# Performance work log

Hardware: AMD Instinct MI355X
Metric: run time of the kernel (lower is better)

## Reference

```python
import jax, jax.numpy as jnp
import numpy as np

N_NODES = 100000


def gcn_conv(x, src, dst, w, W, b, n):
    # PyG GCNConv: add self loops (weight 1), symmetric normalization,
    # linear transform, scatter-add aggregation, bias.
    loop = jnp.arange(n, dtype=src.dtype)
    s = jnp.concatenate([src, loop])
    d = jnp.concatenate([dst, loop])
    ew = jnp.concatenate([w, jnp.ones((n,), dtype=w.dtype)])
    deg = jax.ops.segment_sum(ew, d, num_segments=n)          # [N]
    dinv = jnp.where(deg > 0, jax.lax.rsqrt(deg), 0.0).astype(x.dtype)
    norm = dinv[s] * ew * dinv[d]                             # [E+N]
    h = x @ W                                                 # [N, out]
    msg = h[s] * norm[:, None]                                # gather + scale
    out = jax.ops.segment_sum(msg, d, num_segments=n)         # scatter-add
    return out + b


def setup_inputs() -> dict:
    key = jax.random.key(0)
    k1, k2, k3, k4, k5, k6 = jax.random.split(key, 6)
    n, e, c_in, c_hid, c_out = N_NODES, 1200000, 64, 64, 32
    node_matrix = jax.random.normal(k1, (n, c_in), dtype=jnp.float32)
    edge_index = jax.random.randint(k2, (2, e), 0, n, dtype=jnp.int64)
    edge_weights = jax.random.uniform(k3, (e,), dtype=jnp.float32)
    s_in = 1.0 / np.sqrt(c_in)
    s_hid = 1.0 / np.sqrt(c_hid)
    W1 = jax.random.uniform(k4, (c_in, c_hid), jnp.float32, -s_in, s_in)
    b1 = jnp.zeros((c_hid,), jnp.float32)
    W2 = jax.random.uniform(k5, (c_hid, c_out), jnp.float32, -s_hid, s_hid)
    b2 = jnp.zeros((c_out,), jnp.float32)
    return {"node_matrix": node_matrix, "edge_index": edge_index,
            "edge_weights": edge_weights, "W1": W1, "b1": b1, "W2": W2, "b2": b2}


def reference(node_matrix, edge_index, edge_weights, W1, b1, W2, b2):
    n = node_matrix.shape[0]
    src, dst = edge_index[0], edge_index[1]
    x = gcn_conv(node_matrix, src, dst, edge_weights, W1, b1, n)
    x = jax.nn.relu(x)
    x = gcn_conv(x, src, dst, edge_weights, W2, b2, n)
    return x
```

## Files before the change

kernel.cpp:

```cpp
#include <hip/hip_runtime.h>

static inline int ceil_div(long long a, long long b) { return (int)((a + b - 1) / b); }

#define RBITS 8
#define RNODES 256
#define CNT_BLOCKS 96
#define STAGE_CAP 4096

typedef __attribute__((ext_vector_type(8))) short bf16x8;
typedef __attribute__((ext_vector_type(4))) float f32x4;

__device__ inline unsigned f2bf(float f) {
    unsigned u = __float_as_uint(f);
    return (u + 0x7fffu + ((u >> 16) & 1u)) >> 16;
}
__device__ inline unsigned pack2(float a, float b) { return f2bf(a) | (f2bf(b) << 16); }
__device__ inline float bf2f(unsigned v) { return __uint_as_float(v << 16); }
__device__ inline float bf_lo(unsigned v) { return __uint_as_float(v << 16); }
__device__ inline float bf_hi(unsigned v) { return __uint_as_float(v & 0xffff0000u); }

__global__ void bin_count(const int* __restrict__ dst, int* __restrict__ hist_g,
                          int NB, int E) {
    __shared__ int hist[512];
    int t = threadIdx.x;
    hist[t] = 0;
    __syncthreads();
    int nvec = E >> 2;
    const int4* d4 = (const int4*)dst;
    for (int v = blockIdx.x * 512 + t; v < nvec; v += CNT_BLOCKS * 512) {
        int4 d = d4[v];
        atomicAdd(&hist[d.x >> RBITS], 1);
        atomicAdd(&hist[d.y >> RBITS], 1);
        atomicAdd(&hist[d.z >> RBITS], 1);
        atomicAdd(&hist[d.w >> RBITS], 1);
    }
    if (blockIdx.x == 0 && t < (E & 3))
        atomicAdd(&hist[dst[(nvec << 2) + t] >> RBITS], 1);
    __syncthreads();
    if (t < NB) hist_g[blockIdx.x * NB + t] = hist[t];
}

__global__ void bin_scan(const int* __restrict__ hist_g, int* __restrict__ bin_start,
                         int* __restrict__ bin_cursor, int NB) {
    __shared__ int s[512];
    int t = threadIdx.x;
    int v = 0;
    if (t < NB) {
        for (int k = 0; k < CNT_BLOCKS; ++k) v += hist_g[k * NB + t];
        bin_cursor[t] = 0;
    }
    s[t] = v;
    __syncthreads();
    for (int d = 1; d < 512; d <<= 1) {
        int a = (t >= d) ? s[t - d] : 0;
        __syncthreads();
        s[t] += a;
        __syncthreads();
    }
    if (t < NB) bin_start[t] = s[t] - v;
    if (t == NB - 1) bin_start[NB] = s[t];
}

#define SC_T 512
#define SC_K 8
#define SC_E (SC_T * SC_K)
__global__ void bin_scatter(const int* __restrict__ src, const int* __restrict__ dst,
                            const float* __restrict__ w, int* __restrict__ bin_cursor,
                            const int* __restrict__ bin_start,
                            int* __restrict__ bp, float* __restrict__ bw,
                            int NB, int E) {
    __shared__ int hist[512];
    __shared__ int offs[512];
    __shared__ int base[512];
    __shared__ int stage_p[SC_E];
    __shared__ float stage_w[SC_E];
    __shared__ unsigned short stage_b[SC_E];
    int t = threadIdx.x;
    hist[t] = 0;
    __syncthreads();
    int e0 = blockIdx.x * SC_E;
    int nE = E - e0; if (nE > SC_E) nE = SC_E;

    int myBin[SC_K], myRank[SC_K], myPack[SC_K];
    float myW[SC_K];
#pragma unroll
    for (int k = 0; k < SC_K; ++k) {
        int idx = t + k * SC_T;
        if (idx < nE) {
            int e = e0 + idx;
            int d = dst[e];
            int b = d >> RBITS;
            myBin[k] = b;
            myPack[k] = (src[e] << RBITS) | (d & (RNODES - 1));
            myW[k] = w[e];
            myRank[k] = atomicAdd(&hist[b], 1);
        }
    }
    __syncthreads();
    offs[t] = hist[t];
    __syncthreads();
    for (int d = 1; d < 512; d <<= 1) {
        int a = (t >= d) ? offs[t - d] : 0;
        __syncthreads();
        offs[t] += a;
        __syncthreads();
    }
    if (t < NB && hist[t]) base[t] = bin_start[t] + atomicAdd(&bin_cursor[t], hist[t]);
#pragma unroll
    for (int k = 0; k < SC_K; ++k) {
        int idx = t + k * SC_T;
        if (idx < nE) {
            int b = myBin[k];
            int pos = (offs[b] - hist[b]) + myRank[k];
            stage_p[pos] = myPack[k];
            stage_w[pos] = myW[k];
            stage_b[pos] = (unsigned short)b;
        }
    }
    __syncthreads();
    for (int p = t; p < nE; p += SC_T) {
        int b = stage_b[p];
        int g = base[b] + (p - (offs[b] - hist[b]));
        bp[g] = stage_p[p];
        bw[g] = stage_w[p];
    }
}

__global__ void csr_build(const int* __restrict__ bp, const float* __restrict__ bw,
                          const int* __restrict__ bin_start,
                          int* __restrict__ row_beg, int* __restrict__ row_cnt,
                          float* __restrict__ dinv, unsigned* __restrict__ ew, int N) {
    __shared__ int cnt[RNODES];
    __shared__ float wsum[RNODES];
    __shared__ int starts[RNODES];
    __shared__ int cur[RNODES];
    __shared__ int sp[STAGE_CAP];
    __shared__ float sw[STAGE_CAP];
    int b = blockIdx.x;
    int t = threadIdx.x;
    if (t < RNODES) { cnt[t] = 0; wsum[t] = 0.f; }
    __syncthreads();
    int beg = bin_start[b], end = bin_start[b + 1];
    int n = end - beg;
    for (int idx = t; idx < n; idx += 512) {
        int p = bp[beg + idx];
        float wv = bw[beg + idx];
        if (idx < STAGE_CAP) { sp[idx] = p; sw[idx] = wv; }
        atomicAdd(&cnt[p & (RNODES - 1)], 1);
        atomicAdd(&wsum[p & (RNODES - 1)], wv);
    }
    __syncthreads();
    if (t < RNODES) starts[t] = cnt[t];
    __syncthreads();
    for (int d = 1; d < RNODES; d <<= 1) {
        int a = 0;
        if (t < RNODES && t >= d) a = starts[t - d];
        __syncthreads();
        if (t < RNODES) starts[t] += a;
        __syncthreads();
    }
    if (t < RNODES) {
        int ex = starts[t] - cnt[t];
        cur[t] = beg + ex;
        int node = (b << RBITS) + t;
        if (node < N) {
            row_beg[node] = beg + ex;
            row_cnt[node] = cnt[t];
            dinv[node] = rsqrtf(wsum[t] + 1.0f);
        }
    }
    __syncthreads();
    for (int idx = t; idx < n; idx += 512) {
        int p;
        float wv;
        if (idx < STAGE_CAP) { p = sp[idx]; wv = sw[idx]; }
        else { p = bp[beg + idx]; wv = bw[beg + idx]; }
        int slot = atomicAdd(&cur[p & (RNODES - 1)], 1);
        ew[slot] = ((unsigned)(p >> RBITS) << 15) | (f2bf(wv) & 0x7fffu);
    }
}

__global__ __launch_bounds__(256) void gemm1_mfma(const float* __restrict__ X,
                                                  const float* __restrict__ W,
                                                  const float* __restrict__ dinv,
                                                  unsigned short* __restrict__ H, int N) {
    int lane = threadIdx.x & 63;
    int wv = threadIdx.x >> 6;
    int quad = lane >> 4;
    int col = lane & 15;

    bf16x8 Bh[4][2], Bl[4][2];
#pragma unroll
    for (int nt = 0; nt < 4; ++nt)
#pragma unroll
        for (int kh = 0; kh < 2; ++kh)
#pragma unroll
            for (int j = 0; j < 8; ++j) {
                float wval = W[(kh * 32 + quad * 8 + j) * 64 + nt * 16 + col];
                unsigned hb = f2bf(wval);
                Bh[nt][kh][j] = (short)hb;
                Bl[nt][kh][j] = (short)f2bf(wval - bf2f(hb));
            }

#pragma unroll
    for (int rt = 0; rt < 4; ++rt) {
        int rb = blockIdx.x * 256 + wv * 64 + rt * 16;
        if (rb >= N) break;
        int arow = rb + col;
        bf16x8 Ah[2], Al[2];
#pragma unroll
        for (int kh = 0; kh < 2; ++kh) {
            float xv[8];
            if (arow < N) {
                const float4* p = (const float4*)(X + (size_t)arow * 64 + kh * 32 + quad * 8);
                float4 f0 = p[0], f1 = p[1];
                xv[0] = f0.x; xv[1] = f0.y; xv[2] = f0.z; xv[3] = f0.w;
                xv[4] = f1.x; xv[5] = f1.y; xv[6] = f1.z; xv[7] = f1.w;
            } else {
#pragma unroll
                for (int j = 0; j < 8; ++j) xv[j] = 0.f;
            }
#pragma unroll
            for (int j = 0; j < 8; ++j) {
                unsigned hb = f2bf(xv[j]);
                Ah[kh][j] = (short)hb;
                Al[kh][j] = (short)f2bf(xv[j] - bf2f(hb));
            }
        }
        f32x4 acc[4] = {{0,0,0,0},{0,0,0,0},{0,0,0,0},{0,0,0,0}};
#pragma unroll
        for (int nt = 0; nt < 4; ++nt)
#pragma unroll
            for (int kh = 0; kh < 2; ++kh) {
                acc[nt] = __builtin_amdgcn_mfma_f32_16x16x32_bf16(Ah[kh], Bh[nt][kh], acc[nt], 0, 0, 0);
                acc[nt] = __builtin_amdgcn_mfma_f32_16x16x32_bf16(Al[kh], Bh[nt][kh], acc[nt], 0, 0, 0);
                acc[nt] = __builtin_amdgcn_mfma_f32_16x16x32_bf16(Ah[kh], Bl[nt][kh], acc[nt], 0, 0, 0);
            }
        float dval[4];
#pragma unroll
        for (int r = 0; r < 4; ++r) {
            int row = rb + quad * 4 + r;
            dval[r] = (row < N) ? dinv[row] : 0.f;
        }
#pragma unroll
        for (int nt = 0; nt < 4; ++nt)
#pragma unroll
            for (int r = 0; r < 4; ++r) {
                int row = rb + quad * 4 + r;
                if (row < N)
                    H[(size_t)row * 64 + nt * 16 + col] = (unsigned short)f2bf(acc[nt][r] * dval[r]);
            }
    }
}

__global__ __launch_bounds__(256) void gemm2_mfma(const unsigned short* __restrict__ Xb,
                                                  const float* __restrict__ W,
                                                  const float* __restrict__ dinv,
                                                  unsigned short* __restrict__ H, int N) {
    int lane = threadIdx.x & 63;
    int wv = threadIdx.x >> 6;
    int quad = lane >> 4;
    int col = lane & 15;

    bf16x8 Bh[2][2], Bl[2][2];
#pragma unroll
    for (int nt = 0; nt < 2; ++nt)
#pragma unroll
        for (int kh = 0; kh < 2; ++kh)
#pragma unroll
            for (int j = 0; j < 8; ++j) {
                float wval = W[(kh * 32 + quad * 8 + j) * 32 + nt * 16 + col];
                unsigned hb = f2bf(wval);
                Bh[nt][kh][j] = (short)hb;
                Bl[nt][kh][j] = (short)f2bf(wval - bf2f(hb));
            }

#pragma unroll
    for (int rt = 0; rt < 4; ++rt) {
        int rb = blockIdx.x * 256 + wv * 64 + rt * 16;
        if (rb >= N) break;
        int arow = rb + col;
        bf16x8 A[2];
#pragma unroll
        for (int kh = 0; kh < 2; ++kh) {
            if (arow < N) {
                const bf16x8* p = (const bf16x8*)(Xb + (size_t)arow * 64 + kh * 32 + quad * 8);
                A[kh] = *p;
            } else {
                A[kh] = bf16x8{0,0,0,0,0,0,0,0};
            }
        }
        f32x4 acc[2] = {{0,0,0,0},{0,0,0,0}};
#pragma unroll
        for (int nt = 0; nt < 2; ++nt)
#pragma unroll
            for (int kh = 0; kh < 2; ++kh) {
                acc[nt] = __builtin_amdgcn_mfma_f32_16x16x32_bf16(A[kh], Bh[nt][kh], acc[nt], 0, 0, 0);
                acc[nt] = __builtin_amdgcn_mfma_f32_16x16x32_bf16(A[kh], Bl[nt][kh], acc[nt], 0, 0, 0);
            }
        float dval[4];
#pragma unroll
        for (int r = 0; r < 4; ++r) {
            int row = rb + quad * 4 + r;
            dval[r] = (row < N) ? dinv[row] : 0.f;
        }
#pragma unroll
        for (int nt = 0; nt < 2; ++nt)
#pragma unroll
            for (int r = 0; r < 4; ++r) {
                int row = rb + quad * 4 + r;
                if (row < N)
                    H[(size_t)row * 32 + nt * 16 + col] = (unsigned short)f2bf(acc[nt][r] * dval[r]);
            }
    }
}

__global__ void aggregate64(const unsigned* __restrict__ g, const int* __restrict__ row_beg,
                            const int* __restrict__ row_cnt, const unsigned* __restrict__ ew,
                            const float* __restrict__ dinv, const float* __restrict__ b,
                            unsigned* __restrict__ outb, int N) {
    int t = threadIdx.x;
    int c = t & 7;
    int i = blockIdx.x * 64 + (t >> 3);
    if (i >= N) return;
    int e = row_beg[i];
    int end = e + row_cnt[i];
    const uint4* h4 = (const uint4*)g;
    float acc[8];
#pragma unroll
    for (int j = 0; j < 8; ++j) acc[j] = 0.f;
    for (; e + 3 < end; e += 4) {
        unsigned e0 = ew[e], e1 = ew[e + 1], e2 = ew[e + 2], e3 = ew[e + 3];
        float n0 = __uint_as_float((e0 & 0x7fffu) << 16);
        float n1 = __uint_as_float((e1 & 0x7fffu) << 16);
        float n2 = __uint_as_float((e2 & 0x7fffu) << 16);
        float n3 = __uint_as_float((e3 & 0x7fffu) << 16);
        uint4 v0 = h4[(size_t)(e0 >> 15) * 8 + c];
        uint4 v1 = h4[(size_t)(e1 >> 15) * 8 + c];
        uint4 v2 = h4[(size_t)(e2 >> 15) * 8 + c];
        uint4 v3 = h4[(size_t)(e3 >> 15) * 8 + c];
        acc[0] += n0 * bf_lo(v0.x) + n1 * bf_lo(v1.x) + n2 * bf_lo(v2.x) + n3 * bf_lo(v3.x);
        acc[1] += n0 * bf_hi(v0.x) + n1 * bf_hi(v1.x) + n2 * bf_hi(v2.x) + n3 * bf_hi(v3.x);
        acc[2] += n0 * bf_lo(v0.y) + n1 * bf_lo(v1.y) + n2 * bf_lo(v2.y) + n3 * bf_lo(v3.y);
        acc[3] += n0 * bf_hi(v0.y) + n1 * bf_hi(v1.y) + n2 * bf_hi(v2.y) + n3 * bf_hi(v3.y);
        acc[4] += n0 * bf_lo(v0.z) + n1 * bf_lo(v1.z) + n2 * bf_lo(v2.z) + n3 * bf_lo(v3.z);
        acc[5] += n0 * bf_hi(v0.z) + n1 * bf_hi(v1.z) + n2 * bf_hi(v2.z) + n3 * bf_hi(v3.z);
        acc[6] += n0 * bf_lo(v0.w) + n1 * bf_lo(v1.w) + n2 * bf_lo(v2.w) + n3 * bf_lo(v3.w);
        acc[7] += n0 * bf_hi(v0.w) + n1 * bf_hi(v1.w) + n2 * bf_hi(v2.w) + n3 * bf_hi(v3.w);
    }
    for (; e < end; ++e) {
        unsigned e0 = ew[e];
        float n0 = __uint_as_float((e0 & 0x7fffu) << 16);
        uint4 v0 = h4[(size_t)(e0 >> 15) * 8 + c];
        acc[0] += n0 * bf_lo(v0.x);
        acc[1] += n0 * bf_hi(v0.x);
        acc[2] += n0 * bf_lo(v0.y);
        acc[3] += n0 * bf_hi(v0.y);
        acc[4] += n0 * bf_lo(v0.z);
        acc[5] += n0 * bf_hi(v0.z);
        acc[6] += n0 * bf_lo(v0.w);
        acc[7] += n0 * bf_hi(v0.w);
    }
    float di = dinv[i];
    uint4 hv = h4[(size_t)i * 8 + c];
    float hs[8] = {bf_lo(hv.x), bf_hi(hv.x), bf_lo(hv.y), bf_hi(hv.y),
                   bf_lo(hv.z), bf_hi(hv.z), bf_lo(hv.w), bf_hi(hv.w)};
    float4 b0 = ((const float4*)b)[c * 2];
    float4 b1 = ((const float4*)b)[c * 2 + 1];
    float o[8];
    o[0] = b0.x + di * (hs[0] + acc[0]);
    o[1] = b0.y + di * (hs[1] + acc[1]);
    o[2] = b0.z + di * (hs[2] + acc[2]);
    o[3] = b0.w + di * (hs[3] + acc[3]);
    o[4] = b1.x + di * (hs[4] + acc[4]);
    o[5] = b1.y + di * (hs[5] + acc[5]);
    o[6] = b1.z + di * (hs[6] + acc[6]);
    o[7] = b1.w + di * (hs[7] + acc[7]);
#pragma unroll
    for (int j = 0; j < 8; ++j) o[j] = fmaxf(o[j], 0.f);
    uint4 ov;
    ov.x = pack2(o[0], o[1]);
    ov.y = pack2(o[2], o[3]);
    ov.z = pack2(o[4], o[5]);
    ov.w = pack2(o[6], o[7]);
    ((uint4*)outb)[(size_t)i * 8 + c] = ov;
}

__global__ void aggregate32(const unsigned* __restrict__ g, const int* __restrict__ row_beg,
                            const int* __restrict__ row_cnt, const unsigned* __restrict__ ew,
                            const float* __restrict__ dinv, const float* __restrict__ b,
                            float* __restrict__ out, int N) {
    int t = threadIdx.x;
    int c = t & 3;
    int i = blockIdx.x * 128 + (t >> 2);
    if (i >= N) return;
    int e = row_beg[i];
    int end = e + row_cnt[i];
    const uint4* h4 = (const uint4*)g;
    float acc[8];
#pragma unroll
    for (int j = 0; j < 8; ++j) acc[j] = 0.f;
    for (; e + 3 < end; e += 4) {
        unsigned e0 = ew[e], e1 = ew[e + 1], e2 = ew[e + 2], e3 = ew[e + 3];
        float n0 = __uint_as_float((e0 & 0x7fffu) << 16);
        float n1 = __uint_as_float((e1 & 0x7fffu) << 16);
        float n2 = __uint_as_float((e2 & 0x7fffu) << 16);
        float n3 = __uint_as_float((e3 & 0x7fffu) << 16);
        uint4 v0 = h4[(size_t)(e0 >> 15) * 4 + c];
        uint4 v1 = h4[(size_t)(e1 >> 15) * 4 + c];
        uint4 v2 = h4[(size_t)(e2 >> 15) * 4 + c];
        uint4 v3 = h4[(size_t)(e3 >> 15) * 4 + c];
        acc[0] += n0 * bf_lo(v0.x) + n1 * bf_lo(v1.x) + n2 * bf_lo(v2.x) + n3 * bf_lo(v3.x);
        acc[1] += n0 * bf_hi(v0.x) + n1 * bf_hi(v1.x) + n2 * bf_hi(v2.x) + n3 * bf_hi(v3.x);
        acc[2] += n0 * bf_lo(v0.y) + n1 * bf_lo(v1.y) + n2 * bf_lo(v2.y) + n3 * bf_lo(v3.y);
        acc[3] += n0 * bf_hi(v0.y) + n1 * bf_hi(v1.y) + n2 * bf_hi(v2.y) + n3 * bf_hi(v3.y);
        acc[4] += n0 * bf_lo(v0.z) + n1 * bf_lo(v1.z) + n2 * bf_lo(v2.z) + n3 * bf_lo(v3.z);
        acc[5] += n0 * bf_hi(v0.z) + n1 * bf_hi(v1.z) + n2 * bf_hi(v2.z) + n3 * bf_hi(v3.z);
        acc[6] += n0 * bf_lo(v0.w) + n1 * bf_lo(v1.w) + n2 * bf_lo(v2.w) + n3 * bf_lo(v3.w);
        acc[7] += n0 * bf_hi(v0.w) + n1 * bf_hi(v1.w) + n2 * bf_hi(v2.w) + n3 * bf_hi(v3.w);
    }
    for (; e < end; ++e) {
        unsigned e0 = ew[e];
        float n0 = __uint_as_float((e0 & 0x7fffu) << 16);
        uint4 v0 = h4[(size_t)(e0 >> 15) * 4 + c];
        acc[0] += n0 * bf_lo(v0.x);
        acc[1] += n0 * bf_hi(v0.x);
        acc[2] += n0 * bf_lo(v0.y);
        acc[3] += n0 * bf_hi(v0.y);
        acc[4] += n0 * bf_lo(v0.z);
        acc[5] += n0 * bf_hi(v0.z);
        acc[6] += n0 * bf_lo(v0.w);
        acc[7] += n0 * bf_hi(v0.w);
    }
    float di = dinv[i];
    uint4 hv = h4[(size_t)i * 4 + c];
    float hs[8] = {bf_lo(hv.x), bf_hi(hv.x), bf_lo(hv.y), bf_hi(hv.y),
                   bf_lo(hv.z), bf_hi(hv.z), bf_lo(hv.w), bf_hi(hv.w)};
    float4 b0 = ((const float4*)b)[c * 2];
    float4 b1 = ((const float4*)b)[c * 2 + 1];
    float4 o0, o1;
    o0.x = b0.x + di * (hs[0] + acc[0]);
    o0.y = b0.y + di * (hs[1] + acc[1]);
    o0.z = b0.z + di * (hs[2] + acc[2]);
    o0.w = b0.w + di * (hs[3] + acc[3]);
    o1.x = b1.x + di * (hs[4] + acc[4]);
    o1.y = b1.y + di * (hs[5] + acc[5]);
    o1.z = b1.z + di * (hs[6] + acc[6]);
    o1.w = b1.w + di * (hs[7] + acc[7]);
    float4* op = (float4*)(out + (size_t)i * 32 + c * 8);
    op[0] = o0;
    op[1] = o1;
}

extern "C" void kernel_launch(void* const* d_in, const int* in_sizes, int n_in,
                              void* d_out, int out_size, void* d_ws, size_t ws_size,
                              hipStream_t stream) {
    const float* x  = (const float*)d_in[0];
    const int* eidx = (const int*)d_in[1];
    const float* w  = (const float*)d_in[2];
    const float* W1 = (const float*)d_in[3];
    const float* b1 = (const float*)d_in[4];
    const float* W2 = (const float*)d_in[5];
    const float* b2 = (const float*)d_in[6];
    float* out = (float*)d_out;

    const int E = in_sizes[2];
    const int N = in_sizes[0] / 64;
    const int* src = eidx;
    const int* dst = eidx + E;
    const int NB = ceil_div(N, RNODES);

    char* ws = (char*)d_ws;
    size_t off = 0;
    auto alloc = [&](size_t bytes) -> void* {
        void* p = ws + off;
        off = (off + bytes + 255) & ~(size_t)255;
        return p;
    };
    int*      hist_g     = (int*)alloc((size_t)CNT_BLOCKS * NB * 4);
    int*      bin_cursor = (int*)alloc((size_t)NB * 4);
    int*      bin_start  = (int*)alloc((size_t)(NB + 1) * 4);
    int*      bp         = (int*)alloc((size_t)E * 4);
    float*    bw         = (float*)alloc((size_t)E * 4);
    unsigned* ew         = (unsigned*)alloc((size_t)E * 4);
    int*      row_beg    = (int*)alloc((size_t)N * 4);
    int*      row_cnt    = (int*)alloc((size_t)N * 4);
    float*    dinv       = (float*)alloc((size_t)N * 4);
    unsigned* g1         = (unsigned*)alloc((size_t)N * 32 * 4);
    unsigned* out1b      = (unsigned*)alloc((size_t)N * 32 * 4);
    unsigned* g2         = (unsigned*)alloc((size_t)N * 16 * 4);

    bin_count<<<CNT_BLOCKS, 512, 0, stream>>>(dst, hist_g, NB, E);
    bin_scan<<<1, 512, 0, stream>>>(hist_g, bin_start, bin_cursor, NB);
    bin_scatter<<<ceil_div(E, SC_E), SC_T, 0, stream>>>(src, dst, w, bin_cursor, bin_start,
                                                        bp, bw, NB, E);
    csr_build<<<NB, 512, 0, stream>>>(bp, bw, bin_start, row_beg, row_cnt, dinv, ew, N);

    gemm1_mfma<<<ceil_div(N, 256), 256, 0, stream>>>(x, W1, dinv, (unsigned short*)g1, N);
    aggregate64<<<ceil_div(N, 64), 512, 0, stream>>>(g1, row_beg, row_cnt, ew, dinv, b1, out1b, N);

    gemm2_mfma<<<ceil_div(N, 256), 256, 0, stream>>>((const unsigned short*)out1b, W2, dinv,
                                                     (unsigned short*)g2, N);
    aggregate32<<<ceil_div(N, 128), 512, 0, stream>>>(g2, row_beg, row_cnt, ew, dinv, b2, out, N);
}
```

Baseline: 204.3 us.

## Process two nodes per thread group in aggregation kernels; drop csr_build LDS staging

Both aggregation kernels now assign two destination rows to each thread group and interleave their edge loops, issuing eight independent gathers per iteration instead of four. The aim is more memory-level parallelism to hide gather latency, at the cost of half as many launched threads and more registers. Separately, csr_build drops its shared-memory staging of bin entries and re-reads bp/bw from global memory in the second pass, which frees LDS and may raise occupancy but adds global traffic.

```diff
diff --git a/kernel.cpp b/kernel.cpp
--- a/kernel.cpp
+++ b/kernel.cpp
@@ -5,7 +5,6 @@
 #define RBITS 8
 #define RNODES 256
 #define CNT_BLOCKS 96
-#define STAGE_CAP 4096
 
 typedef __attribute__((ext_vector_type(8))) short bf16x8;
 typedef __attribute__((ext_vector_type(4))) float f32x4;
@@ -18,6 +17,20 @@
 __device__ inline float bf2f(unsigned v) { return __uint_as_float(v << 16); }
 __device__ inline float bf_lo(unsigned v) { return __uint_as_float(v << 16); }
 __device__ inline float bf_hi(unsigned v) { return __uint_as_float(v & 0xffff0000u); }
+
+#define ACC8(acc, n, v)                      \
+    do {                                     \
+        acc[0] += (n) * bf_lo((v).x);        \
+        acc[1] += (n) * bf_hi((v).x);        \
+        acc[2] += (n) * bf_lo((v).y);        \
+        acc[3] += (n) * bf_hi((v).y);        \
+        acc[4] += (n) * bf_lo((v).z);        \
+        acc[5] += (n) * bf_hi((v).z);        \
+        acc[6] += (n) * bf_lo((v).w);        \
+        acc[7] += (n) * bf_hi((v).w);        \
+    } while (0)
+
+#define EWN(e) __uint_as_float(((e) & 0x7fffu) << 16)
 
 __global__ void bin_count(const int* __restrict__ dst, int* __restrict__ hist_g,
                           int NB, int E) {
@@ -134,20 +147,15 @@
     __shared__ float wsum[RNODES];
     __shared__ int starts[RNODES];
     __shared__ int cur[RNODES];
-    __shared__ int sp[STAGE_CAP];
-    __shared__ float sw[STAGE_CAP];
     int b = blockIdx.x;
     int t = threadIdx.x;
     if (t < RNODES) { cnt[t] = 0; wsum[t] = 0.f; }
     __syncthreads();
     int beg = bin_start[b], end = bin_start[b + 1];
-    int n = end - beg;
-    for (int idx = t; idx < n; idx += 512) {
-        int p = bp[beg + idx];
-        float wv = bw[beg + idx];
-        if (idx < STAGE_CAP) { sp[idx] = p; sw[idx] = wv; }
+    for (int e = beg + t; e < end; e += 512) {
+        int p = bp[e];
         atomicAdd(&cnt[p & (RNODES - 1)], 1);
-        atomicAdd(&wsum[p & (RNODES - 1)], wv);
+        atomicAdd(&wsum[p & (RNODES - 1)], bw[e]);
     }
     __syncthreads();
     if (t < RNODES) starts[t] = cnt[t];
@@ -170,13 +178,10 @@
         }
     }
     __syncthreads();
-    for (int idx = t; idx < n; idx += 512) {
-        int p;
-        float wv;
-        if (idx < STAGE_CAP) { p = sp[idx]; wv = sw[idx]; }
-        else { p = bp[beg + idx]; wv = bw[beg + idx]; }
+    for (int e = beg + t; e < end; e += 512) {
+        int p = bp[e];
         int slot = atomicAdd(&cur[p & (RNODES - 1)], 1);
-        ew[slot] = ((unsigned)(p >> RBITS) << 15) | (f2bf(wv) & 0x7fffu);
+        ew[slot] = ((unsigned)(p >> RBITS) << 15) | (f2bf(bw[e]) & 0x7fffu);
     }
 }
 
@@ -321,69 +326,102 @@
                             unsigned* __restrict__ outb, int N) {
     int t = threadIdx.x;
     int c = t & 7;
-    int i = blockIdx.x * 64 + (t >> 3);
-    if (i >= N) return;
-    int e = row_beg[i];
-    int end = e + row_cnt[i];
+    int i0 = blockIdx.x * 128 + (t >> 3) * 2;
+    if (i0 >= N) return;
+    int i1 = i0 + 1;
+    bool hasB = i1 < N;
+    int eA = row_beg[i0], endA = eA + row_cnt[i0];
+    int eB = hasB ? row_beg[i1] : 0;
+    int endB = hasB ? eB + row_cnt[i1] : 0;
     const uint4* h4 = (const uint4*)g;
-    float acc[8];
-#pragma unroll
-    for (int j = 0; j < 8; ++j) acc[j] = 0.f;
-    for (; e + 3 < end; e += 4) {
-        unsigned e0 = ew[e], e1 = ew[e + 1], e2 = ew[e + 2], e3 = ew[e + 3];
-        float n0 = __uint_as_float((e0 & 0x7fffu) << 16);
-        float n1 = __uint_as_float((e1 & 0x7fffu) << 16);
-        float n2 = __uint_as_float((e2 & 0x7fffu) << 16);
-        float n3 = __uint_as_float((e3 & 0x7fffu) << 16);
-        uint4 v0 = h4[(size_t)(e0 >> 15) * 8 + c];
-        uint4 v1 = h4[(size_t)(e1 >> 15) * 8 + c];
-        uint4 v2 = h4[(size_t)(e2 >> 15) * 8 + c];
-        uint4 v3 = h4[(size_t)(e3 >> 15) * 8 + c];
-        acc[0] += n0 * bf_lo(v0.x) + n1 * bf_lo(v1.x) + n2 * bf_lo(v2.x) + n3 * bf_lo(v3.x);
-        acc[1] += n0 * bf_hi(v0.x) + n1 * bf_hi(v1.x) + n2 * bf_hi(v2.x) + n3 * bf_hi(v3.x);
-        acc[2] += n0 * bf_lo(v0.y) + n1 * bf_lo(v1.y) + n2 * bf_lo(v2.y) + n3 * bf_lo(v3.y);
-        acc[3] += n0 * bf_hi(v0.y) + n1 * bf_hi(v1.y) + n2 * bf_hi(v2.y) + n3 * bf_hi(v3.y);
-        acc[4] += n0 * bf_lo(v0.z) + n1 * bf_lo(v1.z) + n2 * bf_lo(v2.z) + n3 * bf_lo(v3.z);
-        acc[5] += n0 * bf_hi(v0.z) + n1 * bf_hi(v1.z) + n2 * bf_hi(v2.z) + n3 * bf_hi(v3.z);
-        acc[6] += n0 * bf_lo(v0.w) + n1 * bf_lo(v1.w) + n2 * bf_lo(v2.w) + n3 * bf_lo(v3.w);
-        acc[7] += n0 * bf_hi(v0.w) + n1 * bf_hi(v1.w) + n2 * bf_hi(v2.w) + n3 * bf_hi(v3.w);
-    }
-    for (; e < end; ++e) {
-        unsigned e0 = ew[e];
-        float n0 = __uint_as_float((e0 & 0x7fffu) << 16);
-        uint4 v0 = h4[(size_t)(e0 >> 15) * 8 + c];
-        acc[0] += n0 * bf_lo(v0.x);
-        acc[1] += n0 * bf_hi(v0.x);
-        acc[2] += n0 * bf_lo(v0.y);
-        acc[3] += n0 * bf_hi(v0.y);
-        acc[4] += n0 * bf_lo(v0.z);
-        acc[5] += n0 * bf_hi(v0.z);
-        acc[6] += n0 * bf_lo(v0.w);
-        acc[7] += n0 * bf_hi(v0.w);
-    }
-    float di = dinv[i];
-    uint4 hv = h4[(size_t)i * 8 + c];
-    float hs[8] = {bf_lo(hv.x), bf_hi(hv.x), bf_lo(hv.y), bf_hi(hv.y),
-                   bf_lo(hv.z), bf_hi(hv.z), bf_lo(hv.w), bf_hi(hv.w)};
-    float4 b0 = ((const float4*)b)[c * 2];
-    float4 b1 = ((const float4*)b)[c * 2 + 1];
-    float o[8];
-    o[0] = b0.x + di * (hs[0] + acc[0]);
-    o[1] = b0.y + di * (hs[1] + acc[1]);
-    o[2] = b0.z + di * (hs[2] + acc[2]);
-    o[3] = b0.w + di * (hs[3] + acc[3]);
-    o[4] = b1.x + di * (hs[4] + acc[4]);
-    o[5] = b1.y + di * (hs[5] + acc[5]);
-    o[6] = b1.z + di * (hs[6] + acc[6]);
-    o[7] = b1.w + di * (hs[7] + acc[7]);
-#pragma unroll
-    for (int j = 0; j < 8; ++j) o[j] = fmaxf(o[j], 0.f);
-    uint4 ov;
-    ov.x = pack2(o[0], o[1]);
-    ov.y = pack2(o[2], o[3]);
-    ov.z = pack2(o[4], o[5]);
-    ov.w = pack2(o[6], o[7]);
-    ((uint4*)outb)[(size_t)i * 8 + c] = ov;
+    float accA[8], accB[8];
+#pragma unroll
+    for (int j = 0; j < 8; ++j) { accA[j] = 0.f; accB[j] = 0.f; }
+    while (eA + 3 < endA && eB + 3 < endB) {
+        unsigned a0 = ew[eA], a1 = ew[eA + 1], a2 = ew[eA + 2], a3 = ew[eA + 3];
+        unsigned b0 = ew[eB], b1 = ew[eB + 1], b2 = ew[eB + 2], b3 = ew[eB + 3];
+        uint4 va0 = h4[(size_t)(a0 >> 15) * 8 + c];
+        uint4 va1 = h4[(size_t)(a1 >> 15) * 8 + c];
+        uint4 va2 = h4[(size_t)(a2 >> 15) * 8 + c];
+        uint4 va3 = h4[(size_t)(a3 >> 15) * 8 + c];
+        uint4 vb0 = h4[(size_t)(b0 >> 15) * 8 + c];
+        uint4 vb1 = h4[(size_t)(b1 >> 15) * 8 + c];
+        uint4 vb2 = h4[(size_t)(b2 >> 15) * 8 + c];
+        uint4 vb3 = h4[(size_t)(b3 >> 15) * 8 + c];
+        ACC8(accA, EWN(a0), va0); ACC8(accA, EWN(a1), va1);
+        ACC8(accA, EWN(a2), va2); ACC8(accA, EWN(a3), va3);
+        ACC8(accB, EWN(b0), vb0); ACC8(accB, EWN(b1), vb1);
+        ACC8(accB, EWN(b2), vb2); ACC8(accB, EWN(b3), vb3);
+        eA += 4; eB += 4;
+    }
+    for (; eA + 3 < endA; eA += 4) {
+        unsigned a0 = ew[eA], a1 = ew[eA + 1], a2 = ew[eA + 2], a3 = ew[eA + 3];
+        uint4 va0 = h4[(size_t)(a0 >> 15) * 8 + c];
+        uint4 va1 = h4[(size_t)(a1 >> 15) * 8 + c];
+        uint4 va2 = h4[(size_t)(a2 >> 15) * 8 + c];
+        uint4 va3 = h4[(size_t)(a3 >> 15) * 8 + c];
+        ACC8(accA, EWN(a0), va0); ACC8(accA, EWN(a1), va1);
+        ACC8(accA, EWN(a2), va2); ACC8(accA, EWN(a3), va3);
+    }
+    for (; eA < endA; ++eA) {
+        unsigned a0 = ew[eA];
+        uint4 va0 = h4[(size_t)(a0 >> 15) * 8 + c];
+        ACC8(accA, EWN(a0), va0);
+    }
+    for (; eB + 3 < endB; eB += 4) {
+        unsigned b0 = ew[eB], b1 = ew[eB + 1], b2 = ew[eB + 2], b3 = ew[eB + 3];
+        uint4 vb0 = h4[(size_t)(b0 >> 15) * 8 + c];
+        uint4 vb1 = h4[(size_t)(b1 >> 15) * 8 + c];
+        uint4 vb2 = h4[(size_t)(b2 >> 15) * 8 + c];
+        uint4 vb3 = h4[(size_t)(b3 >> 15) * 8 + c];
+        ACC8(accB, EWN(b0), vb0); ACC8(accB, EWN(b1), vb1);
+        ACC8(accB, EWN(b2), vb2); ACC8(accB, EWN(b3), vb3);
+    }
+    for (; eB < endB; ++eB) {
+        unsigned b0 = ew[eB];
+        uint4 vb0 = h4[(size_t)(b0 >> 15) * 8 + c];
+        ACC8(accB, EWN(b0), vb0);
+    }
+    const float4* b4 = (const float4*)b;
+    float4 bv0 = b4[c * 2];
+    float4 bv1 = b4[c * 2 + 1];
+    float bb[8] = {bv0.x, bv0.y, bv0.z, bv0.w, bv1.x, bv1.y, bv1.z, bv1.w};
+    {
+        float di = dinv[i0];
+        uint4 hv = h4[(size_t)i0 * 8 + c];
+        float hs[8] = {bf_lo(hv.x), bf_hi(hv.x), bf_lo(hv.y), bf_hi(hv.y),
+                       bf_lo(hv.z), bf_hi(hv.z), bf_lo(hv.w), bf_hi(hv.w)};
+        uint4 ov;
+        float o0 = fmaxf(bb[0] + di * (hs[0] + accA[0]), 0.f);
+        float o1 = fmaxf(bb[1] + di * (hs[1] + accA[1]), 0.f);
+        float o2 = fmaxf(bb[2] + di * (hs[2] + accA[2]), 0.f);
+        float o3 = fmaxf(bb[3] + di * (hs[3] + accA[3]), 0.f);
+        float o4 = fmaxf(bb[4] + di * (hs[4] + accA[4]), 0.f);
+        float o5 = fmaxf(bb[5] + di * (hs[5] + accA[5]), 0.f);
+        float o6 = fmaxf(bb[6] + di * (hs[6] + accA[6]), 0.f);
+        float o7 = fmaxf(bb[7] + di * (hs[7] + accA[7]), 0.f);
+        ov.x = pack2(o0, o1); ov.y = pack2(o2, o3);
+        ov.z = pack2(o4, o5); ov.w = pack2(o6, o7);
+        ((uint4*)outb)[(size_t)i0 * 8 + c] = ov;
+    }
+    if (hasB) {
+        float di = dinv[i1];
+        uint4 hv = h4[(size_t)i1 * 8 + c];
+        float hs[8] = {bf_lo(hv.x), bf_hi(hv.x), bf_lo(hv.y), bf_hi(hv.y),
+                       bf_lo(hv.z), bf_hi(hv.z), bf_lo(hv.w), bf_hi(hv.w)};
+        uint4 ov;
+        float o0 = fmaxf(bb[0] + di * (hs[0] + accB[0]), 0.f);
+        float o1 = fmaxf(bb[1] + di * (hs[1] + accB[1]), 0.f);
+        float o2 = fmaxf(bb[2] + di * (hs[2] + accB[2]), 0.f);
+        float o3 = fmaxf(bb[3] + di * (hs[3] + accB[3]), 0.f);
+        float o4 = fmaxf(bb[4] + di * (hs[4] + accB[4]), 0.f);
+        float o5 = fmaxf(bb[5] + di * (hs[5] + accB[5]), 0.f);
+        float o6 = fmaxf(bb[6] + di * (hs[6] + accB[6]), 0.f);
+        float o7 = fmaxf(bb[7] + di * (hs[7] + accB[7]), 0.f);
+        ov.x = pack2(o0, o1); ov.y = pack2(o2, o3);
+        ov.z = pack2(o4, o5); ov.w = pack2(o6, o7);
+        ((uint4*)outb)[(size_t)i1 * 8 + c] = ov;
+    }
 }
 
 __global__ void aggregate32(const unsigned* __restrict__ g, const int* __restrict__ row_beg,
@@ -392,64 +430,102 @@
                             float* __restrict__ out, int N) {
     int t = threadIdx.x;
     int c = t & 3;
-    int i = blockIdx.x * 128 + (t >> 2);
-    if (i >= N) return;
-    int e = row_beg[i];
-    int end = e + row_cnt[i];
+    int i0 = blockIdx.x * 256 + (t >> 2) * 2;
+    if (i0 >= N) return;
+    int i1 = i0 + 1;
+    bool hasB = i1 < N;
+    int eA = row_beg[i0], endA = eA + row_cnt[i0];
+    int eB = hasB ? row_beg[i1] : 0;
+    int endB = hasB ? eB + row_cnt[i1] : 0;
     const uint4* h4 = (const uint4*)g;
-    float acc[8];
-#pragma unroll
-    for (int j = 0; j < 8; ++j) acc[j] = 0.f;
-    for (; e + 3 < end; e += 4) {
-        unsigned e0 = ew[e], e1 = ew[e + 1], e2 = ew[e + 2], e3 = ew[e + 3];
-        float n0 = __uint_as_float((e0 & 0x7fffu) << 16);
-        float n1 = __uint_as_float((e1 & 0x7fffu) << 16);
-        float n2 = __uint_as_float((e2 & 0x7fffu) << 16);
-        float n3 = __uint_as_float((e3 & 0x7fffu) << 16);
-        uint4 v0 = h4[(size_t)(e0 >> 15) * 4 + c];
-        uint4 v1 = h4[(size_t)(e1 >> 15) * 4 + c];
-        uint4 v2 = h4[(size_t)(e2 >> 15) * 4 + c];
-        uint4 v3 = h4[(size_t)(e3 >> 15) * 4 + c];
-        acc[0] += n0 * bf_lo(v0.x) + n1 * bf_lo(v1.x) + n2 * bf_lo(v2.x) + n3 * bf_lo(v3.x);
-        acc[1] += n0 * bf_hi(v0.x) + n1 * bf_hi(v1.x) + n2 * bf_hi(v2.x) + n3 * bf_hi(v3.x);
-        acc[2] += n0 * bf_lo(v0.y) + n1 * bf_lo(v1.y) + n2 * bf_lo(v2.y) + n3 * bf_lo(v3.y);
-        acc[3] += n0 * bf_hi(v0.y) + n1 * bf_hi(v1.y) + n2 * bf_hi(v2.y) + n3 * bf_hi(v3.y);
-        acc[4] += n0 * bf_lo(v0.z) + n1 * bf_lo(v1.z) + n2 * bf_lo(v2.z) + n3 * bf_lo(v3.z);
-        acc[5] += n0 * bf_hi(v0.z) + n1 * bf_hi(v1.z) + n2 * bf_hi(v2.z) + n3 * bf_hi(v3.z);
-        acc[6] += n0 * bf_lo(v0.w) + n1 * bf_lo(v1.w) + n2 * bf_lo(v2.w) + n3 * bf_lo(v3.w);
-        acc[7] += n0 * bf_hi(v0.w) + n1 * bf_hi(v1.w) + n2 * bf_hi(v2.w) + n3 * bf_hi(v3.w);
-    }
-    for (; e < end; ++e) {
-        unsigned e0 = ew[e];
-        float n0 = __uint_as_float((e0 & 0x7fffu) << 16);
-        uint4 v0 = h4[(size_t)(e0 >> 15) * 4 + c];
-        acc[0] += n0 * bf_lo(v0.x);
-        acc[1] += n0 * bf_hi(v0.x);
-        acc[2] += n0 * bf_lo(v0.y);
-        acc[3] += n0 * bf_hi(v0.y);
-        acc[4] += n0 * bf_lo(v0.z);
-        acc[5] += n0 * bf_hi(v0.z);
-        acc[6] += n0 * bf_lo(v0.w);
-        acc[7] += n0 * bf_hi(v0.w);
-    }
-    float di = dinv[i];
-    uint4 hv = h4[(size_t)i * 4 + c];
-    float hs[8] = {bf_lo(hv.x), bf_hi(hv.x), bf_lo(hv.y), bf_hi(hv.y),
-                   bf_lo(hv.z), bf_hi(hv.z), bf_lo(hv.w), bf_hi(hv.w)};
-    float4 b0 = ((const float4*)b)[c * 2];
-    float4 b1 = ((const float4*)b)[c * 2 + 1];
-    float4 o0, o1;
-    o0.x = b0.x + di * (hs[0] + acc[0]);
-    o0.y = b0.y + di * (hs[1] + acc[1]);
-    o0.z = b0.z + di * (hs[2] + acc[2]);
-    o0.w = b0.w + di * (hs[3] + acc[3]);
-    o1.x = b1.x + di * (hs[4] + acc[4]);
-    o1.y = b1.y + di * (hs[5] + acc[5]);
-    o1.z = b1.z + di * (hs[6] + acc[6]);
-    o1.w = b1.w + di * (hs[7] + acc[7]);
-    float4* op = (float4*)(out + (size_t)i * 32 + c * 8);
-    op[0] = o0;
-    op[1] = o1;
+    float accA[8], accB[8];
+#pragma unroll
+    for (int j = 0; j < 8; ++j) { accA[j] = 0.f; accB[j] = 0.f; }
+    while (eA + 3 < endA && eB + 3 < endB) {
+        unsigned a0 = ew[eA], a1 = ew[eA + 1], a2 = ew[eA + 2], a3 = ew[eA + 3];
+        unsigned b0 = ew[eB], b1 = ew[eB + 1], b2 = ew[eB + 2], b3 = ew[eB + 3];
+        uint4 va0 = h4[(size_t)(a0 >> 15) * 4 + c];
+        uint4 va1 = h4[(size_t)(a1 >> 15) * 4 + c];
+        uint4 va2 = h4[(size_t)(a2 >> 15) * 4 + c];
+        uint4 va3 = h4[(size_t)(a3 >> 15) * 4 + c];
+        uint4 vb0 = h4[(size_t)(b0 >> 15) * 4 + c];
+        uint4 vb1 = h4[(size_t)(b1 >> 15) * 4 + c];
+        uint4 vb2 = h4[(size_t)(b2 >> 15) * 4 + c];
+        uint4 vb3 = h4[(size_t)(b3 >> 15) * 4 + c];
+        ACC8(accA, EWN(a0), va0); ACC8(accA, EWN(a1), va1);
+        ACC8(accA, EWN(a2), va2); ACC8(accA, EWN(a3), va3);
+        ACC8(accB, EWN(b0), vb0); ACC8(accB, EWN(b1), vb1);
+        ACC8(accB, EWN(b2), vb2); ACC8(accB, EWN(b3), vb3);
+        eA += 4; eB += 4;
+    }
+    for (; eA + 3 < endA; eA += 4) {
+        unsigned a0 = ew[eA], a1 = ew[eA + 1], a2 = ew[eA + 2], a3 = ew[eA + 3];
+        uint4 va0 = h4[(size_t)(a0 >> 15) * 4 + c];
+        uint4 va1 = h4[(size_t)(a1 >> 15) * 4 + c];
+        uint4 va2 = h4[(size_t)(a2 >> 15) * 4 + c];
+        uint4 va3 = h4[(size_t)(a3 >> 15) * 4 + c];
+        ACC8(accA, EWN(a0), va0); ACC8(accA, EWN(a1), va1);
+        ACC8(accA, EWN(a2), va2); ACC8(accA, EWN(a3), va3);
+    }
+    for (; eA < endA; ++eA) {
+        unsigned a0 = ew[eA];
+        uint4 va0 = h4[(size_t)(a0 >> 15) * 4 + c];
+        ACC8(accA, EWN(a0), va0);
+    }
+    for (; eB + 3 < endB; eB += 4) {
+        unsigned b0 = ew[eB], b1 = ew[eB + 1], b2 = ew[eB + 2], b3 = ew[eB + 3];
+        uint4 vb0 = h4[(size_t)(b0 >> 15) * 4 + c];
+        uint4 vb1 = h4[(size_t)(b1 >> 15) * 4 + c];
+        uint4 vb2 = h4[(size_t)(b2 >> 15) * 4 + c];
+        uint4 vb3 = h4[(size_t)(b3 >> 15) * 4 + c];
+        ACC8(accB, EWN(b0), vb0); ACC8(accB, EWN(b1), vb1);
+        ACC8(accB, EWN(b2), vb2); ACC8(accB, EWN(b3), vb3);
+    }
+    for (; eB < endB; ++eB) {
+        unsigned b0 = ew[eB];
+        uint4 vb0 = h4[(size_t)(b0 >> 15) * 4 + c];
+        ACC8(accB, EWN(b0), vb0);
+    }
+    const float4* b4 = (const float4*)b;
+    float4 bv0 = b4[c * 2];
+    float4 bv1 = b4[c * 2 + 1];
+    float bb[8] = {bv0.x, bv0.y, bv0.z, bv0.w, bv1.x, bv1.y, bv1.z, bv1.w};
+    {
+        float di = dinv[i0];
+        uint4 hv = h4[(size_t)i0 * 4 + c];
+        float hs[8] = {bf_lo(hv.x), bf_hi(hv.x), bf_lo(hv.y), bf_hi(hv.y),
+                       bf_lo(hv.z), bf_hi(hv.z), bf_lo(hv.w), bf_hi(hv.w)};
+        float4 o0, o1;
+        o0.x = bb[0] + di * (hs[0] + accA[0]);
+        o0.y = bb[1] + di * (hs[1] + accA[1]);
+        o0.z = bb[2] + di * (hs[2] + accA[2]);
+        o0.w = bb[3] + di * (hs[3] + accA[3]);
+        o1.x = bb[4] + di * (hs[4] + accA[4]);
+        o1.y = bb[5] + di * (hs[5] + accA[5]);
+        o1.z = bb[6] + di * (hs[6] + accA[6]);
+        o1.w = bb[7] + di * (hs[7] + accA[7]);
+        float4* op = (float4*)(out + (size_t)i0 * 32 + c * 8);
+        op[0] = o0;
+        op[1] = o1;
+    }
+    if (hasB) {
+        float di = dinv[i1];
+        uint4 hv = h4[(size_t)i1 * 4 + c];
+        float hs[8] = {bf_lo(hv.x), bf_hi(hv.x), bf_lo(hv.y), bf_hi(hv.y),
+                       bf_lo(hv.z), bf_hi(hv.z), bf_lo(hv.w), bf_hi(hv.w)};
+        float4 o0, o1;
+        o0.x = bb[0] + di * (hs[0] + accB[0]);
+        o0.y = bb[1] + di * (hs[1] + accB[1]);
+        o0.z = bb[2] + di * (hs[2] + accB[2]);
+        o0.w = bb[3] + di * (hs[3] + accB[3]);
+        o1.x = bb[4] + di * (hs[4] + accB[4]);
+        o1.y = bb[5] + di * (hs[5] + accB[5]);
+        o1.z = bb[6] + di * (hs[6] + accB[6]);
+        o1.w = bb[7] + di * (hs[7] + accB[7]);
+        float4* op = (float4*)(out + (size_t)i1 * 32 + c * 8);
+        op[0] = o0;
+        op[1] = o1;
+    }
 }
 
 extern "C" void kernel_launch(void* const* d_in, const int* in_sizes, int n_in,
@@ -497,9 +573,9 @@
     csr_build<<<NB, 512, 0, stream>>>(bp, bw, bin_start, row_beg, row_cnt, dinv, ew, N);
 
     gemm1_mfma<<<ceil_div(N, 256), 256, 0, stream>>>(x, W1, dinv, (unsigned short*)g1, N);
-    aggregate64<<<ceil_div(N, 64), 512, 0, stream>>>(g1, row_beg, row_cnt, ew, dinv, b1, out1b, N);
+    aggregate64<<<ceil_div(N, 128), 512, 0, stream>>>(g1, row_beg, row_cnt, ew, dinv, b1, out1b, N);
 
     gemm2_mfma<<<ceil_div(N, 256), 256, 0, stream>>>((const unsigned short*)out1b, W2, dinv,
                                                      (unsigned short*)g2, N);
-    aggregate32<<<ceil_div(N, 128), 512, 0, stream>>>(g2, row_beg, row_cnt, ew, dinv, b2, out, N);
-}
+    aggregate32<<<ceil_div(N, 256), 512, 0, stream>>>(g2, row_beg, row_cnt, ew, dinv, b2, out, N);
+}
```

Measured after the change: 217.0 us. +6.2%, slower.
